# Optimization experiments

Measured on AMD Instinct MI355X. Metric: run time of the kernel, lower is better.

The kernel has to match this reference:

```python
import jax, jax.numpy as jnp
import numpy as np

N, M, D = 8192, 8192, 128
EPS = 1e-9


def setup_inputs() -> dict:
    key = jax.random.key(0)
    k1, k2 = jax.random.split(key)
    X = jax.random.normal(k1, (N, D), dtype=jnp.float32)
    Y = jax.random.normal(k2, (M, D), dtype=jnp.float32)
    sigma = jnp.ones((1,), dtype=jnp.float32)  # bandwidth (self.sigma)
    return {"X": X, "Y": Y, "sigma": sigma}


def reference(X, Y, sigma):
    # l2norm: ||x_i - y_j||^2 = ||x_i||^2 - 2 x_i.y_j + ||y_j||^2
    # (original builds full XX/YY Gram matrices just for their diagonals;
    #  same math via row-wise sums of squares)
    x2 = jnp.sum(X * X, axis=1)          # [n]
    y2 = jnp.sum(Y * Y, axis=1)          # [m]
    xy = jnp.matmul(X, Y.T)              # [n, m]
    dnorm2 = x2[:, None] - 2.0 * xy + y2[None, :]
    sigma2_inv = 1.0 / (sigma[0] ** 2 + EPS)
    K_XY = jnp.exp(-sigma2_inv * dnorm2)  # [n, m]
    return K_XY
```

## Files before the change

### kernel.cpp

```cpp
#include <hip/hip_runtime.h>
#include <stdint.h>

#define D_DIM 128
#define NROW 8192
#define MROW 8192
#define TILE 128
#define LDK2 72
#define OUT_LD 8192

typedef __bf16 bf16x8 __attribute__((ext_vector_type(8)));
typedef float f32x4 __attribute__((ext_vector_type(4)));

__device__ __forceinline__ unsigned short f32_to_bf16(float f) {
    uint32_t u = __float_as_uint(f);
    u = (u + 0x7FFFu + ((u >> 16) & 1u)) >> 16;
    return (unsigned short)u;
}

__global__ __launch_bounds__(256) void rbf_norms(const float* __restrict__ X,
                                                 const float* __restrict__ Y,
                                                 float* __restrict__ nrm) {
    const int t = threadIdx.x;
    const int w = t >> 6, lane = t & 63;
    const int rid = blockIdx.x * 4 + w;
    const float* src = (rid < NROW) ? (X + (size_t)rid * D_DIM)
                                    : (Y + (size_t)(rid - NROW) * D_DIM);
    float2 v = *(const float2*)(src + 2 * lane);
    float s = v.x * v.x + v.y * v.y;
    #pragma unroll
    for (int off = 32; off > 0; off >>= 1) s += __shfl_xor(s, off, 64);
    if (lane == 0) nrm[rid] = s;
}

__global__ __launch_bounds__(256, 4) void rbf_main(const float* __restrict__ X,
                                                   const float* __restrict__ Y,
                                                   const float* __restrict__ sigma,
                                                   const float* __restrict__ nrm,
                                                   float* __restrict__ out) {
    __shared__ unsigned short Xs[TILE][LDK2];
    __shared__ unsigned short Ys[TILE][LDK2];
    __shared__ float x2s[TILE];
    __shared__ float y2s[TILE];

    const int t = threadIdx.x;
    const int row0 = blockIdx.y * TILE;
    const int col0 = blockIdx.x * TILE;

    if (t < 128) x2s[t] = nrm[row0 + t];
    else         y2s[t - 128] = nrm[NROW + col0 + (t - 128)];

    const int w = t >> 6, ln = t & 63;
    const int quad = ln >> 4, l16 = ln & 15;
    const int wr = (w >> 1) * 64;
    const int wc = (w & 1) * 64;

    f32x4 acc[4][4] = {};

    #pragma unroll
    for (int p = 0; p < 2; ++p) {
        #pragma unroll
        for (int i = 0; i < 8; ++i) {
            int f = t + 256 * i;
            int r = f >> 4;
            int c = (f & 15) * 4;
            float4 vx = *(const float4*)(X + (size_t)(row0 + r) * D_DIM + p * 64 + c);
            float4 vy = *(const float4*)(Y + (size_t)(col0 + r) * D_DIM + p * 64 + c);
            ushort4 hx = { f32_to_bf16(vx.x), f32_to_bf16(vx.y), f32_to_bf16(vx.z), f32_to_bf16(vx.w) };
            ushort4 hy = { f32_to_bf16(vy.x), f32_to_bf16(vy.y), f32_to_bf16(vy.z), f32_to_bf16(vy.w) };
            *(ushort4*)(&Xs[r][c]) = hx;
            *(ushort4*)(&Ys[r][c]) = hy;
        }
        __syncthreads();

        #pragma unroll
        for (int ks = 0; ks < 2; ++ks) {
            const int k = ks * 32 + quad * 8;
            bf16x8 ax[4], by[4];
            #pragma unroll
            for (int ti = 0; ti < 4; ++ti)
                ax[ti] = *(const bf16x8*)(&Xs[wr + ti * 16 + l16][k]);
            #pragma unroll
            for (int tj = 0; tj < 4; ++tj)
                by[tj] = *(const bf16x8*)(&Ys[wc + tj * 16 + l16][k]);
            #pragma unroll
            for (int ti = 0; ti < 4; ++ti)
                #pragma unroll
                for (int tj = 0; tj < 4; ++tj)
                    acc[ti][tj] = __builtin_amdgcn_mfma_f32_16x16x32_bf16(by[tj], ax[ti], acc[ti][tj], 0, 0, 0);
        }
        if (p == 0) __syncthreads();
    }

    const float s2 = sigma[0] * sigma[0] + 1e-9f;
    const float cexp = -1.4426950408889634f / s2;

    float x2r[4];
    #pragma unroll
    for (int ti = 0; ti < 4; ++ti) x2r[ti] = x2s[wr + ti * 16 + l16];

    #pragma unroll
    for (int tj = 0; tj < 4; ++tj) {
        f32x4 y2v = *(const f32x4*)(&y2s[wc + tj * 16 + quad * 4]);
        size_t gcol = (size_t)(col0 + wc + tj * 16 + quad * 4);
        #pragma unroll
        for (int ti = 0; ti < 4; ++ti) {
            f32x4 v;
            #pragma unroll
            for (int r = 0; r < 4; ++r) {
                float d = x2r[ti] + y2v[r] - 2.0f * acc[ti][tj][r];
                v[r] = __builtin_amdgcn_exp2f(d * cexp);
            }
            size_t grow = (size_t)(row0 + wr + ti * 16 + l16);
            __builtin_nontemporal_store(v, (f32x4*)(out + grow * OUT_LD + gcol));
        }
    }
}

extern "C" void kernel_launch(void* const* d_in, const int* in_sizes, int n_in,
                              void* d_out, int out_size, void* d_ws, size_t ws_size,
                              hipStream_t stream) {
    const float* X = (const float*)d_in[0];
    const float* Y = (const float*)d_in[1];
    const float* sigma = (const float*)d_in[2];
    float* nrm = (float*)d_ws;
    float* out = (float*)d_out;

    rbf_norms<<<(NROW + MROW) / 4, 256, 0, stream>>>(X, Y, nrm);
    rbf_main<<<dim3(MROW / TILE, NROW / TILE), 256, 0, stream>>>(X, Y, sigma, nrm, out);
}
```

Measured before the change: 309.6 us.

## Prepack inputs to swizzled bf16 tiles and load via global_load_lds

Adds a pre-pass kernel that converts X and Y to bf16 once and writes them in a tile-ordered, XOR-swizzled layout. The main kernel then copies these tiles straight into LDS with global_load_lds, which removes the per-tile fp32 loads and bf16 conversions and the padded LDS layout. The block-to-tile mapping is remapped across XCDs, and the output stores change from nontemporal to regular stores. The cost is an extra kernel launch and a workspace pass over the inputs; the store change may affect cache behaviour on the 256MB output.

```diff
diff --git a/kernel.cpp b/kernel.cpp
--- a/kernel.cpp
+++ b/kernel.cpp
@@ -5,11 +5,12 @@
 #define NROW 8192
 #define MROW 8192
 #define TILE 128
-#define LDK2 72
 #define OUT_LD 8192
+#define NTILE 64
 
 typedef __bf16 bf16x8 __attribute__((ext_vector_type(8)));
 typedef float f32x4 __attribute__((ext_vector_type(4)));
+typedef unsigned short u16x8 __attribute__((ext_vector_type(8)));
 
 __device__ __forceinline__ unsigned short f32_to_bf16(float f) {
     uint32_t u = __float_as_uint(f);
@@ -32,19 +33,46 @@
     if (lane == 0) nrm[rid] = s;
 }
 
-__global__ __launch_bounds__(256, 4) void rbf_main(const float* __restrict__ X,
-                                                   const float* __restrict__ Y,
+__global__ __launch_bounds__(256) void rbf_pack(const float* __restrict__ X,
+                                                const float* __restrict__ Y,
+                                                unsigned short* __restrict__ Xt,
+                                                unsigned short* __restrict__ Yt) {
+    const int gid = blockIdx.x * 256 + threadIdx.x;
+    const int mat = gid >> 17;
+    const int u = gid & 131071;
+    const int chunk = u >> 10;
+    const int b16 = u & 1023;
+    const int tt = chunk >> 1, p = chunk & 1;
+    const int r = b16 >> 3;
+    const int k2 = (((b16 & 7) << 4) ^ ((r & 7) << 4));
+    const int k = k2 >> 1;
+    const float* src = (mat ? Y : X) + (size_t)(tt * TILE + r) * D_DIM + p * 64 + k;
+    float4 a = *(const float4*)src;
+    float4 b = *(const float4*)(src + 4);
+    u16x8 h = { f32_to_bf16(a.x), f32_to_bf16(a.y), f32_to_bf16(a.z), f32_to_bf16(a.w),
+                f32_to_bf16(b.x), f32_to_bf16(b.y), f32_to_bf16(b.z), f32_to_bf16(b.w) };
+    unsigned short* dst = (mat ? Yt : Xt) + (size_t)chunk * 8192 + (size_t)b16 * 8;
+    *(u16x8*)dst = h;
+}
+
+__global__ __launch_bounds__(256, 4) void rbf_main(const unsigned short* __restrict__ Xt,
+                                                   const unsigned short* __restrict__ Yt,
                                                    const float* __restrict__ sigma,
                                                    const float* __restrict__ nrm,
                                                    float* __restrict__ out) {
-    __shared__ unsigned short Xs[TILE][LDK2];
-    __shared__ unsigned short Ys[TILE][LDK2];
+    __shared__ unsigned short Xs[8192];
+    __shared__ unsigned short Ys[8192];
     __shared__ float x2s[TILE];
     __shared__ float y2s[TILE];
 
     const int t = threadIdx.x;
-    const int row0 = blockIdx.y * TILE;
-    const int col0 = blockIdx.x * TILE;
+
+    const int flat = blockIdx.y * 64 + blockIdx.x;
+    const int nf = (flat & 7) * 512 + (flat >> 3);
+    const int tyi = nf >> 6;
+    const int txi = nf & 63;
+    const int row0 = tyi * TILE;
+    const int col0 = txi * TILE;
 
     if (t < 128) x2s[t] = nrm[row0 + t];
     else         y2s[t - 128] = nrm[NROW + col0 + (t - 128)];
@@ -53,35 +81,40 @@
     const int quad = ln >> 4, l16 = ln & 15;
     const int wr = (w >> 1) * 64;
     const int wc = (w & 1) * 64;
+    const int xorv = (l16 & 7) << 4;
 
     f32x4 acc[4][4] = {};
 
     #pragma unroll
     for (int p = 0; p < 2; ++p) {
+        const char* gx = (const char*)Xt + ((size_t)(tyi * 2 + p) << 14);
+        const char* gy = (const char*)Yt + ((size_t)(txi * 2 + p) << 14);
         #pragma unroll
-        for (int i = 0; i < 8; ++i) {
-            int f = t + 256 * i;
-            int r = f >> 4;
-            int c = (f & 15) * 4;
-            float4 vx = *(const float4*)(X + (size_t)(row0 + r) * D_DIM + p * 64 + c);
-            float4 vy = *(const float4*)(Y + (size_t)(col0 + r) * D_DIM + p * 64 + c);
-            ushort4 hx = { f32_to_bf16(vx.x), f32_to_bf16(vx.y), f32_to_bf16(vx.z), f32_to_bf16(vx.w) };
-            ushort4 hy = { f32_to_bf16(vy.x), f32_to_bf16(vy.y), f32_to_bf16(vy.z), f32_to_bf16(vy.w) };
-            *(ushort4*)(&Xs[r][c]) = hx;
-            *(ushort4*)(&Ys[r][c]) = hy;
+        for (int i = 0; i < 4; ++i) {
+            const int off = ((w * 4 + i) * 64 + ln) * 16;
+            const int loff = (w * 4 + i) * 1024;
+            __builtin_amdgcn_global_load_lds(
+                (const __attribute__((address_space(1))) unsigned int*)(gx + off),
+                (__attribute__((address_space(3))) unsigned int*)((char*)Xs + loff),
+                16, 0, 0);
+            __builtin_amdgcn_global_load_lds(
+                (const __attribute__((address_space(1))) unsigned int*)(gy + off),
+                (__attribute__((address_space(3))) unsigned int*)((char*)Ys + loff),
+                16, 0, 0);
         }
+        asm volatile("s_waitcnt vmcnt(0)" ::: "memory");
         __syncthreads();
 
         #pragma unroll
         for (int ks = 0; ks < 2; ++ks) {
-            const int k = ks * 32 + quad * 8;
+            const int kb = (((ks << 6) | (quad << 4)) ^ xorv);
             bf16x8 ax[4], by[4];
             #pragma unroll
             for (int ti = 0; ti < 4; ++ti)
-                ax[ti] = *(const bf16x8*)(&Xs[wr + ti * 16 + l16][k]);
+                ax[ti] = *(const bf16x8*)((const char*)Xs + (wr + ti * 16 + l16) * 128 + kb);
             #pragma unroll
             for (int tj = 0; tj < 4; ++tj)
-                by[tj] = *(const bf16x8*)(&Ys[wc + tj * 16 + l16][k]);
+                by[tj] = *(const bf16x8*)((const char*)Ys + (wc + tj * 16 + l16) * 128 + kb);
             #pragma unroll
             for (int ti = 0; ti < 4; ++ti)
                 #pragma unroll
@@ -111,7 +144,7 @@
                 v[r] = __builtin_amdgcn_exp2f(d * cexp);
             }
             size_t grow = (size_t)(row0 + wr + ti * 16 + l16);
-            __builtin_nontemporal_store(v, (f32x4*)(out + grow * OUT_LD + gcol));
+            *(f32x4*)(out + grow * OUT_LD + gcol) = v;
         }
     }
 }
@@ -123,8 +156,11 @@
     const float* Y = (const float*)d_in[1];
     const float* sigma = (const float*)d_in[2];
     float* nrm = (float*)d_ws;
+    unsigned short* Xt = (unsigned short*)((char*)d_ws + 65536);
+    unsigned short* Yt = Xt + (size_t)128 * 8192;
     float* out = (float*)d_out;
 
     rbf_norms<<<(NROW + MROW) / 4, 256, 0, stream>>>(X, Y, nrm);
-    rbf_main<<<dim3(MROW / TILE, NROW / TILE), 256, 0, stream>>>(X, Y, sigma, nrm, out);
+    rbf_pack<<<1024, 256, 0, stream>>>(X, Y, Xt, Yt);
+    rbf_main<<<dim3(MROW / TILE, NROW / TILE), 256, 0, stream>>>(Xt, Yt, sigma, nrm, out);
 }
```

Result: faster. 282.0 us (-8.9%).
